# Optimization experiments

Hardware: AMD Instinct MI355X
Metric: run time of the kernel (lower is better)

## Reference

```python
import jax, jax.numpy as jnp
import numpy as np

NEG = -1000000.0  # mask fill value used by the torch module


def setup_inputs() -> dict:
    key = jax.random.key(0)
    k1, k2, k3, k4 = jax.random.split(key, 4)
    B, L, D = 64, 1024, 64
    return {
        "queries": jax.random.normal(k1, (B, L, D), dtype=jnp.float32),
        "keys": jax.random.normal(k2, (B, L, D), dtype=jnp.float32),
        "values": jax.random.normal(k3, (B, L, D), dtype=jnp.float32),
        "valid_lens": jax.random.randint(k4, (B,), 1, 1024, dtype=jnp.int32),
    }


def reference(queries, keys, values, valid_lens):
    d = queries.shape[-1]
    # [B, Lq, Lk] attention scores
    scores = jnp.einsum("bqd,bkd->bqk", queries, keys) / jnp.sqrt(jnp.asarray(d, queries.dtype))
    Lk = scores.shape[-1]
    # sequence mask: key positions >= valid_len are filled with NEG (per batch)
    col = jnp.arange(Lk)  # [Lk]
    mask = col[None, None, :] >= valid_lens[:, None, None]  # [B, 1, Lk] -> broadcasts over q
    scores = jnp.where(mask, NEG, scores)
    attn = jax.nn.softmax(scores, axis=-1)
    # dropout p=0.0 (eval) -> identity
    return jnp.einsum("bqk,bkd->bqd", attn, values)
```

## Files before the change

kernel.cpp:

```cpp
#include <hip/hip_runtime.h>
#include <math.h>


typedef __attribute__((ext_vector_type(4))) float f32x4;
typedef __attribute__((ext_vector_type(8))) short bf16x8;
typedef __attribute__((ext_vector_type(4))) unsigned int u32x4;

constexpr int Bn = 64, Ln = 1024, Dn = 64;
constexpr int NITEM = Bn * 16;
constexpr int NBLK = 768;
constexpr float QSCALE = 0.125f * 1.44269504088896340736f;
constexpr float DEFER_THR = 10.0f;

__device__ inline unsigned int cvt_pk(float lo, float hi) {
    unsigned int r;
    asm("v_cvt_pk_bf16_f32 %0, %1, %2" : "=v"(r) : "v"(lo), "v"(hi));
    return r;
}

__global__ __launch_bounds__(64) void setup_queue(const int* __restrict__ VL,
                                                  int* __restrict__ ws)
{
    const int l = threadIdx.x;
    const int vme = VL[l];
    int rank = 0;
    for (int i = 0; i < 64; ++i) {
        const int vi = __shfl(vme, i, 64);
        rank += (vi > vme) || (vi == vme && i < l);
    }
    ws[1 + rank] = l;
    if (l == 0) ws[0] = NBLK;
}

__global__ __launch_bounds__(256) void flash_attn(
    const float* __restrict__ Q, const float* __restrict__ K,
    const float* __restrict__ V, const int* __restrict__ VL,
    float* __restrict__ O, int* __restrict__ ws)
{
    __shared__ unsigned short kls[2][64 * 64];
    __shared__ unsigned short vls[2][64 * 64];
    __shared__ int bcast;

    const int tid = threadIdx.x;
    const int w = tid >> 6, l = tid & 63;
    const int lg = l >> 4, ln = l & 15;

    const int* ord = ws + 1;
    int* ctr = ws;

    const int kr = tid >> 2, kc = (tid & 3) * 16;
    const int sr = (kr & 0x23) | ((kr & 0x04) << 2) | ((kr & 0x18) >> 1);
    const int vd = l, vk0 = w * 16;

    char* const kls0 = reinterpret_cast<char*>(kls[0]);
    char* const kls1 = reinterpret_cast<char*>(kls[1]);
    char* const vls0 = reinterpret_cast<char*>(vls[0]);
    char* const vls1 = reinterpret_cast<char*>(vls[1]);

    const int kb = sr * 128 + kc * 2, ksw = (sr & 7) << 4;
    const int vb = vd * 128 + vk0 * 2, vsw = (vd & 7) << 4;

    f32x4 kpre[4];
    float vpre[16];

    auto stage_write = [&](int pbuf) {
        char* kd = pbuf ? kls1 : kls0;
        char* vdst = pbuf ? vls1 : vls0;
        u32x4 c;
        c[0] = cvt_pk(kpre[0][0], kpre[0][1]);
        c[1] = cvt_pk(kpre[0][2], kpre[0][3]);
        c[2] = cvt_pk(kpre[1][0], kpre[1][1]);
        c[3] = cvt_pk(kpre[1][2], kpre[1][3]);
        *reinterpret_cast<u32x4*>(kd + ((kb)      ^ ksw)) = c;
        c[0] = cvt_pk(kpre[2][0], kpre[2][1]);
        c[1] = cvt_pk(kpre[2][2], kpre[2][3]);
        c[2] = cvt_pk(kpre[3][0], kpre[3][1]);
        c[3] = cvt_pk(kpre[3][2], kpre[3][3]);
        *reinterpret_cast<u32x4*>(kd + ((kb + 16) ^ ksw)) = c;
        c[0] = cvt_pk(vpre[0],  vpre[1]);
        c[1] = cvt_pk(vpre[2],  vpre[3]);
        c[2] = cvt_pk(vpre[4],  vpre[5]);
        c[3] = cvt_pk(vpre[6],  vpre[7]);
        *reinterpret_cast<u32x4*>(vdst + ((vb)      ^ vsw)) = c;
        c[0] = cvt_pk(vpre[8],  vpre[9]);
        c[1] = cvt_pk(vpre[10], vpre[11]);
        c[2] = cvt_pk(vpre[12], vpre[13]);
        c[3] = cvt_pk(vpre[14], vpre[15]);
        *reinterpret_cast<u32x4*>(vdst + ((vb + 16) ^ vsw)) = c;
    };

    int item = blockIdx.x;

    while (true) {
        const int b = ord[item >> 4];
        const int qt = item & 15;
        const int qbase = qt * 64 + w * 16;
        const int valid = VL[b];
        const int nkt = (valid + 63) >> 6;

        const float* Kbase = K + (size_t)b * Ln * Dn;
        const float* Vbase = V + (size_t)b * Ln * Dn;

        bf16x8 bq0, bq1;
        {
            const f32x4* qp = reinterpret_cast<const f32x4*>(Q + ((size_t)b * Ln + qbase + ln) * Dn);
            f32x4 q0 = qp[lg * 2], q1 = qp[lg * 2 + 1], q2 = qp[8 + lg * 2], q3 = qp[8 + lg * 2 + 1];
            u32x4 c;
            c[0] = cvt_pk(q0[0] * QSCALE, q0[1] * QSCALE);
            c[1] = cvt_pk(q0[2] * QSCALE, q0[3] * QSCALE);
            c[2] = cvt_pk(q1[0] * QSCALE, q1[1] * QSCALE);
            c[3] = cvt_pk(q1[2] * QSCALE, q1[3] * QSCALE);
            bq0 = reinterpret_cast<bf16x8&>(c);
            u32x4 d;
            d[0] = cvt_pk(q2[0] * QSCALE, q2[1] * QSCALE);
            d[1] = cvt_pk(q2[2] * QSCALE, q2[3] * QSCALE);
            d[2] = cvt_pk(q3[0] * QSCALE, q3[1] * QSCALE);
            d[3] = cvt_pk(q3[2] * QSCALE, q3[3] * QSCALE);
            bq1 = reinterpret_cast<bf16x8&>(d);
        }

        {
            const f32x4* kp = reinterpret_cast<const f32x4*>(Kbase + (size_t)kr * Dn + kc);
            #pragma unroll
            for (int i = 0; i < 4; ++i) kpre[i] = kp[i];
            const float* vp = Vbase + (size_t)vk0 * Dn + vd;
            #pragma unroll
            for (int i = 0; i < 16; ++i) vpre[i] = vp[(size_t)i * Dn];
        }
        stage_write(0);
        __syncthreads();

        f32x4 acc[4] = {{0.f,0.f,0.f,0.f},{0.f,0.f,0.f,0.f},{0.f,0.f,0.f,0.f},{0.f,0.f,0.f,0.f}};
        float mrow = -1e30f;
        float lrow = 0.f;

        int p = 0;
        for (int kt = 0; kt < nkt; ++kt, p ^= 1) {
            const bool has_next = (kt + 1 < nkt);
            char* kcur = p ? kls1 : kls0;
            char* vcur = p ? vls1 : vls0;

            if (has_next) {
                const f32x4* kp = reinterpret_cast<const f32x4*>(Kbase + (size_t)((kt + 1) * 64 + kr) * Dn + kc);
                #pragma unroll
                for (int i = 0; i < 4; ++i) kpre[i] = kp[i];
                const float* vp = Vbase + (size_t)((kt + 1) * 64 + vk0) * Dn + vd;
                #pragma unroll
                for (int i = 0; i < 16; ++i) vpre[i] = vp[(size_t)i * Dn];
            }

            f32x4 st[4] = {{0.f,0.f,0.f,0.f},{0.f,0.f,0.f,0.f},{0.f,0.f,0.f,0.f},{0.f,0.f,0.f,0.f}};
            __builtin_amdgcn_s_setprio(1);
            #pragma unroll
            for (int t = 0; t < 4; ++t) {
                const int rr = 16 * t + ln, rsw = (rr & 7) << 4;
                bf16x8 ak0 = *reinterpret_cast<const bf16x8*>(kcur + ((rr * 128 + lg * 16)      ^ rsw));
                st[t] = __builtin_amdgcn_mfma_f32_16x16x32_bf16(ak0, bq0, st[t], 0, 0, 0);
                bf16x8 ak1 = *reinterpret_cast<const bf16x8*>(kcur + ((rr * 128 + lg * 16 + 64) ^ rsw));
                st[t] = __builtin_amdgcn_mfma_f32_16x16x32_bf16(ak1, bq1, st[t], 0, 0, 0);
            }
            __builtin_amdgcn_s_setprio(0);

            if (kt * 64 + 64 > valid) {
                #pragma unroll
                for (int t = 0; t < 4; ++t)
                    #pragma unroll
                    for (int j = 0; j < 4; ++j)
                        if (kt * 64 + 32 * (t >> 1) + 8 * lg + 4 * (t & 1) + j >= valid)
                            st[t][j] = -1e30f;
            }

            float mx;
            {
                float a0 = fmaxf(fmaxf(st[0][0], st[0][1]), fmaxf(st[0][2], st[0][3]));
                float a1 = fmaxf(fmaxf(st[1][0], st[1][1]), fmaxf(st[1][2], st[1][3]));
                float a2 = fmaxf(fmaxf(st[2][0], st[2][1]), fmaxf(st[2][2], st[2][3]));
                float a3 = fmaxf(fmaxf(st[3][0], st[3][1]), fmaxf(st[3][2], st[3][3]));
                mx = fmaxf(fmaxf(a0, a1), fmaxf(a2, a3));
                mx = fmaxf(mx, __shfl_xor(mx, 16, 64));
                mx = fmaxf(mx, __shfl_xor(mx, 32, 64));
            }

            if (__any(mx - mrow > DEFER_THR)) {
                const float mn = fmaxf(mrow, mx);
                const float rs = exp2f(mrow - mn);
                mrow = mn;
                lrow *= rs;
                #pragma unroll
                for (int j = 0; j < 4; ++j) {
                    const float rsj = __shfl(rs, lg * 4 + j, 64);
                    #pragma unroll
                    for (int t = 0; t < 4; ++t) acc[t][j] *= rsj;
                }
            }

            float pv[4][4];
            float rsum = 0.f;
            #pragma unroll
            for (int t = 0; t < 4; ++t)
                #pragma unroll
                for (int j = 0; j < 4; ++j) {
                    pv[t][j] = exp2f(st[t][j] - mrow);
                    rsum += pv[t][j];
                }
            u32x4 w0, w1;
            w0[0] = cvt_pk(pv[0][0], pv[0][1]);  w0[1] = cvt_pk(pv[0][2], pv[0][3]);
            w0[2] = cvt_pk(pv[1][0], pv[1][1]);  w0[3] = cvt_pk(pv[1][2], pv[1][3]);
            w1[0] = cvt_pk(pv[2][0], pv[2][1]);  w1[1] = cvt_pk(pv[2][2], pv[2][3]);
            w1[2] = cvt_pk(pv[3][0], pv[3][1]);  w1[3] = cvt_pk(pv[3][2], pv[3][3]);
            bf16x8 pa0 = reinterpret_cast<bf16x8&>(w0);
            bf16x8 pa1 = reinterpret_cast<bf16x8&>(w1);
            rsum += __shfl_xor(rsum, 16, 64);
            rsum += __shfl_xor(rsum, 32, 64);
            lrow += rsum;

            __builtin_amdgcn_s_setprio(1);
            #pragma unroll
            for (int t = 0; t < 4; ++t) {
                const int rr = 16 * t + ln, rsw = (rr & 7) << 4;
                bf16x8 bv0 = *reinterpret_cast<const bf16x8*>(vcur + ((rr * 128 + lg * 16)      ^ rsw));
                acc[t] = __builtin_amdgcn_mfma_f32_16x16x32_bf16(pa0, bv0, acc[t], 0, 0, 0);
                bf16x8 bv1 = *reinterpret_cast<const bf16x8*>(vcur + ((rr * 128 + lg * 16 + 64) ^ rsw));
                acc[t] = __builtin_amdgcn_mfma_f32_16x16x32_bf16(pa1, bv1, acc[t], 0, 0, 0);
            }
            __builtin_amdgcn_s_setprio(0);

            if (has_next) stage_write(p ^ 1);
            __syncthreads();
        }

        const float invl = 1.0f / lrow;
        float inv[4];
        #pragma unroll
        for (int j = 0; j < 4; ++j) inv[j] = __shfl(invl, lg * 4 + j, 64);
        float* Orow = O + ((size_t)b * Ln + qbase) * Dn;
        #pragma unroll
        for (int t = 0; t < 4; ++t) {
            #pragma unroll
            for (int j = 0; j < 4; ++j) {
                const int q = lg * 4 + j;
                const int d = 16 * t + ln;
                Orow[(size_t)q * Dn + d] = acc[t][j] * inv[j];
            }
        }

        if (tid == 0) bcast = atomicAdd(ctr, 1);
        __syncthreads();
        item = bcast;
        if (item >= NITEM) break;
        __syncthreads();
    }
}

extern "C" void kernel_launch(void* const* d_in, const int* in_sizes, int n_in,
                              void* d_out, int out_size, void* d_ws, size_t ws_size,
                              hipStream_t stream) {
    const float* Q = (const float*)d_in[0];
    const float* K = (const float*)d_in[1];
    const float* V = (const float*)d_in[2];
    const int* VL = (const int*)d_in[3];
    float* O = (float*)d_out;
    int* ws = (int*)d_ws;

    setup_queue<<<1, 64, 0, stream>>>(VL, ws);
    flash_attn<<<NBLK, 256, 0, stream>>>(Q, K, V, VL, O, ws);
}
```

Before: 117.6 us.

## Deepen K/V global prefetch to two tiles ahead with dual register buffers

```diff
diff --git a/kernel.cpp b/kernel.cpp
--- a/kernel.cpp
+++ b/kernel.cpp
@@ -60,35 +60,6 @@
     const int kb = sr * 128 + kc * 2, ksw = (sr & 7) << 4;
     const int vb = vd * 128 + vk0 * 2, vsw = (vd & 7) << 4;
 
-    f32x4 kpre[4];
-    float vpre[16];
-
-    auto stage_write = [&](int pbuf) {
-        char* kd = pbuf ? kls1 : kls0;
-        char* vdst = pbuf ? vls1 : vls0;
-        u32x4 c;
-        c[0] = cvt_pk(kpre[0][0], kpre[0][1]);
-        c[1] = cvt_pk(kpre[0][2], kpre[0][3]);
-        c[2] = cvt_pk(kpre[1][0], kpre[1][1]);
-        c[3] = cvt_pk(kpre[1][2], kpre[1][3]);
-        *reinterpret_cast<u32x4*>(kd + ((kb)      ^ ksw)) = c;
-        c[0] = cvt_pk(kpre[2][0], kpre[2][1]);
-        c[1] = cvt_pk(kpre[2][2], kpre[2][3]);
-        c[2] = cvt_pk(kpre[3][0], kpre[3][1]);
-        c[3] = cvt_pk(kpre[3][2], kpre[3][3]);
-        *reinterpret_cast<u32x4*>(kd + ((kb + 16) ^ ksw)) = c;
-        c[0] = cvt_pk(vpre[0],  vpre[1]);
-        c[1] = cvt_pk(vpre[2],  vpre[3]);
-        c[2] = cvt_pk(vpre[4],  vpre[5]);
-        c[3] = cvt_pk(vpre[6],  vpre[7]);
-        *reinterpret_cast<u32x4*>(vdst + ((vb)      ^ vsw)) = c;
-        c[0] = cvt_pk(vpre[8],  vpre[9]);
-        c[1] = cvt_pk(vpre[10], vpre[11]);
-        c[2] = cvt_pk(vpre[12], vpre[13]);
-        c[3] = cvt_pk(vpre[14], vpre[15]);
-        *reinterpret_cast<u32x4*>(vdst + ((vb + 16) ^ vsw)) = c;
-    };
-
     int item = blockIdx.x;
 
     while (true) {
@@ -100,6 +71,32 @@
 
         const float* Kbase = K + (size_t)b * Ln * Dn;
         const float* Vbase = V + (size_t)b * Ln * Dn;
+
+        auto issue_loads = [&](int t, f32x4 (&kp)[4], float (&vp)[16]) {
+            const f32x4* kpp = reinterpret_cast<const f32x4*>(Kbase + (size_t)(t * 64 + kr) * Dn + kc);
+            #pragma unroll
+            for (int i = 0; i < 4; ++i) kp[i] = kpp[i];
+            const float* vpp = Vbase + (size_t)(t * 64 + vk0) * Dn + vd;
+            #pragma unroll
+            for (int i = 0; i < 16; ++i) vp[i] = vpp[(size_t)i * Dn];
+        };
+        auto stage_write = [&](int pbuf, f32x4 (&kp)[4], float (&vp)[16]) {
+            char* kd = pbuf ? kls1 : kls0;
+            char* vdst = pbuf ? vls1 : vls0;
+            u32x4 c;
+            c[0] = cvt_pk(kp[0][0], kp[0][1]);  c[1] = cvt_pk(kp[0][2], kp[0][3]);
+            c[2] = cvt_pk(kp[1][0], kp[1][1]);  c[3] = cvt_pk(kp[1][2], kp[1][3]);
+            *reinterpret_cast<u32x4*>(kd + ((kb)      ^ ksw)) = c;
+            c[0] = cvt_pk(kp[2][0], kp[2][1]);  c[1] = cvt_pk(kp[2][2], kp[2][3]);
+            c[2] = cvt_pk(kp[3][0], kp[3][1]);  c[3] = cvt_pk(kp[3][2], kp[3][3]);
+            *reinterpret_cast<u32x4*>(kd + ((kb + 16) ^ ksw)) = c;
+            c[0] = cvt_pk(vp[0],  vp[1]);   c[1] = cvt_pk(vp[2],  vp[3]);
+            c[2] = cvt_pk(vp[4],  vp[5]);   c[3] = cvt_pk(vp[6],  vp[7]);
+            *reinterpret_cast<u32x4*>(vdst + ((vb)      ^ vsw)) = c;
+            c[0] = cvt_pk(vp[8],  vp[9]);   c[1] = cvt_pk(vp[10], vp[11]);
+            c[2] = cvt_pk(vp[12], vp[13]);  c[3] = cvt_pk(vp[14], vp[15]);
+            *reinterpret_cast<u32x4*>(vdst + ((vb + 16) ^ vsw)) = c;
+        };
 
         bf16x8 bq0, bq1;
         {
@@ -119,34 +116,26 @@
             bq1 = reinterpret_cast<bf16x8&>(d);
         }
 
-        {
-            const f32x4* kp = reinterpret_cast<const f32x4*>(Kbase + (size_t)kr * Dn + kc);
-            #pragma unroll
-            for (int i = 0; i < 4; ++i) kpre[i] = kp[i];
-            const float* vp = Vbase + (size_t)vk0 * Dn + vd;
-            #pragma unroll
-            for (int i = 0; i < 16; ++i) vpre[i] = vp[(size_t)i * Dn];
-        }
-        stage_write(0);
+        f32x4 kpA[4], kpB[4];
+        float vpA[16], vpB[16];
+        issue_loads(0, kpA, vpA);
+        if (nkt > 1) issue_loads(1, kpB, vpB);
+        stage_write(0, kpA, vpA);
         __syncthreads();
 
         f32x4 acc[4] = {{0.f,0.f,0.f,0.f},{0.f,0.f,0.f,0.f},{0.f,0.f,0.f,0.f},{0.f,0.f,0.f,0.f}};
         float mrow = -1e30f;
         float lrow = 0.f;
 
-        int p = 0;
-        for (int kt = 0; kt < nkt; ++kt, p ^= 1) {
-            const bool has_next = (kt + 1 < nkt);
-            char* kcur = p ? kls1 : kls0;
-            char* vcur = p ? vls1 : vls0;
-
-            if (has_next) {
-                const f32x4* kp = reinterpret_cast<const f32x4*>(Kbase + (size_t)((kt + 1) * 64 + kr) * Dn + kc);
-                #pragma unroll
-                for (int i = 0; i < 4; ++i) kpre[i] = kp[i];
-                const float* vp = Vbase + (size_t)((kt + 1) * 64 + vk0) * Dn + vd;
-                #pragma unroll
-                for (int i = 0; i < 16; ++i) vpre[i] = vp[(size_t)i * Dn];
+        #pragma unroll 2
+        for (int kt = 0; kt < nkt; ++kt) {
+            const bool evn = (kt & 1) == 0;
+            char* kcur = evn ? kls0 : kls1;
+            char* vcur = evn ? vls0 : vls1;
+
+            if (kt + 2 < nkt) {
+                if (evn) issue_loads(kt + 2, kpA, vpA);
+                else     issue_loads(kt + 2, kpB, vpB);
             }
 
             f32x4 st[4] = {{0.f,0.f,0.f,0.f},{0.f,0.f,0.f,0.f},{0.f,0.f,0.f,0.f},{0.f,0.f,0.f,0.f}};
@@ -194,20 +183,20 @@
                 }
             }
 
-            float pv[4][4];
+            float pr[4][4];
             float rsum = 0.f;
             #pragma unroll
             for (int t = 0; t < 4; ++t)
                 #pragma unroll
                 for (int j = 0; j < 4; ++j) {
-                    pv[t][j] = exp2f(st[t][j] - mrow);
-                    rsum += pv[t][j];
+                    pr[t][j] = exp2f(st[t][j] - mrow);
+                    rsum += pr[t][j];
                 }
             u32x4 w0, w1;
-            w0[0] = cvt_pk(pv[0][0], pv[0][1]);  w0[1] = cvt_pk(pv[0][2], pv[0][3]);
-            w0[2] = cvt_pk(pv[1][0], pv[1][1]);  w0[3] = cvt_pk(pv[1][2], pv[1][3]);
-            w1[0] = cvt_pk(pv[2][0], pv[2][1]);  w1[1] = cvt_pk(pv[2][2], pv[2][3]);
-            w1[2] = cvt_pk(pv[3][0], pv[3][1]);  w1[3] = cvt_pk(pv[3][2], pv[3][3]);
+            w0[0] = cvt_pk(pr[0][0], pr[0][1]);  w0[1] = cvt_pk(pr[0][2], pr[0][3]);
+            w0[2] = cvt_pk(pr[1][0], pr[1][1]);  w0[3] = cvt_pk(pr[1][2], pr[1][3]);
+            w1[0] = cvt_pk(pr[2][0], pr[2][1]);  w1[1] = cvt_pk(pr[2][2], pr[2][3]);
+            w1[2] = cvt_pk(pr[3][0], pr[3][1]);  w1[3] = cvt_pk(pr[3][2], pr[3][3]);
             bf16x8 pa0 = reinterpret_cast<bf16x8&>(w0);
             bf16x8 pa1 = reinterpret_cast<bf16x8&>(w1);
             rsum += __shfl_xor(rsum, 16, 64);
@@ -225,7 +214,10 @@
             }
             __builtin_amdgcn_s_setprio(0);
 
-            if (has_next) stage_write(p ^ 1);
+            if (kt + 1 < nkt) {
+                if (evn) stage_write(1, kpB, vpB);
+                else     stage_write(0, kpA, vpA);
+            }
             __syncthreads();
         }
 
```

After: 128.8 us. +9.6%, slower.
